# Optimization experiments

Measured on AMD Instinct MI355X. Metric: run time of the kernel, lower is better.

The kernel has to match this reference:

```python
import jax, jax.numpy as jnp
import numpy as np
from jax import lax

NT, NB, NC = 128, 256, 512
HID, EMB, NCLS, NSTEPS, POSE = 256, 128, 37, 25, 256
RNN_IN = NC + EMB + POSE + 576  # 1472, matches GRUCell input dim


def roi_align_2x2(feat, boxes):
    # feat: [C,H,W] -- image 0 only, faithful to roi_align(features, [coord], (2,2))
    # which assigns all nB boxes to batch element 0.
    # boxes: [nB,4] = (x1,y1,x2,y2), torchvision semantics (aligned=False,
    # spatial_scale=1); sampling_ratio fixed to 1 (one sample per bin center).
    C, H, W = feat.shape
    x1, y1, x2, y2 = boxes[:, 0], boxes[:, 1], boxes[:, 2], boxes[:, 3]
    bw = jnp.maximum(x2 - x1, 1.0) * 0.5  # bin width  (output 2x2)
    bh = jnp.maximum(y2 - y1, 1.0) * 0.5  # bin height
    off = jnp.array([0.5, 1.5], boxes.dtype)
    ys = y1[:, None] + off[None, :] * bh[:, None]            # [nB,2]
    xs = x1[:, None] + off[None, :] * bw[:, None]            # [nB,2]
    yy = jnp.broadcast_to(ys[:, :, None], ys.shape + (2,))   # [nB,2,2]
    xx = jnp.broadcast_to(xs[:, None, :], xs.shape[:1] + (2, 2))
    valid = (yy >= -1.0) & (yy <= H) & (xx >= -1.0) & (xx <= W)
    y = jnp.clip(yy, 0.0, H - 1.0)
    x = jnp.clip(xx, 0.0, W - 1.0)
    y0 = jnp.floor(y); x0 = jnp.floor(x)
    y0i = y0.astype(jnp.int32); x0i = x0.astype(jnp.int32)
    y1i = jnp.minimum(y0i + 1, H - 1); x1i = jnp.minimum(x0i + 1, W - 1)
    ly = y - y0; lx = x - x0; hy = 1.0 - ly; hx = 1.0 - lx
    g = lambda yi, xi: feat[:, yi, xi]                       # [C,nB,2,2]
    val = (g(y0i, x0i) * (hy * hx) + g(y0i, x1i) * (hy * lx)
           + g(y1i, x0i) * (ly * hx) + g(y1i, x1i) * (ly * lx))
    val = jnp.where(valid[None], val, 0.0)                   # [C,nB,2,2]
    return jnp.transpose(val, (1, 0, 2, 3)).reshape(val.shape[1], -1)  # [nB,4C]


def setup_inputs() -> dict:
    key = jax.random.key(0)
    ks = jax.random.split(key, 20)
    s = 0.05
    return {
        "feats": jax.random.normal(ks[0], (NT, NB, NC), jnp.float32),
        "pose": jax.random.normal(ks[1], (NB, POSE, 1, NT), jnp.float32),
        "pyr0": jax.random.normal(ks[2], (NB, 16, 16, 128), jnp.float32),
        "pyr1": jax.random.normal(ks[3], (NB, 64, 8, 64), jnp.float32),
        "pyr2": jax.random.normal(ks[4], (NB, 64, 4, 65), jnp.float32),
        "text_length": jnp.full((NB,), NSTEPS, jnp.int32),
        "text": jax.random.randint(ks[5], (NB * NSTEPS,), 0, NCLS),
        # parameters
        "i2h_w": jax.random.normal(ks[6], (HID, NC)) * s,
        "h2h_w": jax.random.normal(ks[7], (HID, HID)) * s,
        "h2h_b": jnp.zeros((HID,)),
        "score_w": jax.random.normal(ks[8], (HID,)) * s,
        "pose_w": jax.random.normal(ks[9], (4, NC + POSE)) * s,
        "pose_b": jnp.zeros((4,)),
        "gru_w_ih": jax.random.normal(ks[10], (3 * HID, RNN_IN)) * s,
        "gru_w_hh": jax.random.normal(ks[11], (3 * HID, HID)) * s,
        "gru_b_ih": jnp.zeros((3 * HID,)),
        "gru_b_hh": jnp.zeros((3 * HID,)),
        "char_emb": jax.random.normal(ks[12], (NCLS + 1, EMB)),
        "gen_w": jax.random.normal(ks[13], (NCLS, HID)) * s,
        "gen_b": jnp.zeros((NCLS,)),
    }


def reference(feats, pose, pyr0, pyr1, pyr2, text_length, text,
              i2h_w, h2h_w, h2h_b, score_w, pose_w, pose_b,
              gru_w_ih, gru_w_hh, gru_b_ih, gru_b_hh,
              char_emb, gen_w, gen_b):
    nT, nB, nC = feats.shape
    # pose.squeeze(2).permute(2,0,1) -> [nT,nB,POSE]
    pose_t = jnp.transpose(pose[:, :, 0, :], (2, 0, 1))
    feats_cat = jnp.concatenate([feats, pose_t], axis=2)       # [nT,nB,nC+POSE]
    feats_proj = jnp.einsum('tbc,hc->tbh', feats, i2h_w)       # i2h, no bias

    # targets: <start>=0 then text+1 per sample (equal lengths -> reshape)
    tgt = text.reshape(nB, NSTEPS).astype(jnp.int32) + 1
    targets = jnp.concatenate([jnp.zeros((nB, 1), jnp.int32), tgt], axis=1).T  # [NSTEPS+1,nB]

    pyramid = (pyr0, pyr1, pyr2)

    def step(hidden, tgt_row):
        emb = char_emb[tgt_row]                                # [nB,EMB]
        hp = hidden @ h2h_w.T + h2h_b                          # [nB,HID]
        e = jnp.tanh(feats_proj + hp[None]) @ score_w          # [nT,nB]
        alpha = jax.nn.softmax(e, axis=0)
        ctx = jnp.einsum('tbc,tb->bc', feats_cat, alpha)       # [nB,nC+POSE]
        coord = jax.nn.sigmoid(ctx @ pose_w.T + pose_b)        # [nB,4]
        crops = []
        for f in pyramid:
            h, w = f.shape[2], f.shape[3]
            scale = jnp.array([h, w, h, w], coord.dtype)
            coord = coord * scale                              # faithful in-loop rescale
            crops.append(roi_align_2x2(f[0], coord))           # [nB,4*C_i]
        x = jnp.concatenate([ctx, emb] + crops, axis=1)        # [nB,RNN_IN]
        gi = x @ gru_w_ih.T + gru_b_ih
        gh = hidden @ gru_w_hh.T + gru_b_hh
        ir, iz, inn = jnp.split(gi, 3, axis=1)
        hr, hz, hn = jnp.split(gh, 3, axis=1)
        r = jax.nn.sigmoid(ir + hr)
        z = jax.nn.sigmoid(iz + hz)
        n = jnp.tanh(inn + r * hn)
        h_new = (1.0 - z) * n + z * hidden
        return h_new, h_new

    hidden0 = jnp.zeros((nB, HID), feats.dtype)
    _, hs = lax.scan(step, hidden0, targets[:NSTEPS])          # [NSTEPS,nB,HID]
    # re-pack per-sample (equal lengths): [b0 t0..t24, b1 t0..t24, ...]
    new_h = jnp.transpose(hs, (1, 0, 2)).reshape(nB * NSTEPS, HID)
    probs = new_h @ gen_w.T + gen_b                            # [nB*NSTEPS,NCLS]
    return probs
```

## Files before the change

### kernel.cpp

```cpp
#include <hip/hip_runtime.h>
#include <hip/hip_bf16.h>

typedef unsigned short u16;
typedef unsigned int u32;
typedef __attribute__((ext_vector_type(8))) short short8;
typedef __attribute__((ext_vector_type(4))) float floatx4;

#define NT 128
#define NB 256
#define NC 512
#define HID 256
#define EMB 128
#define NCLS 37
#define NSTEPS 25
#define POSEC 256
#define RNN_IN 1472

__device__ __forceinline__ float b2f(u16 u) {
    union { float f; u32 i; } v; v.i = ((u32)u) << 16; return v.f;
}
__device__ __forceinline__ u16 f2b(float f) {
    union { float f; u32 i; } v; v.f = f;
    u32 x = v.i;
    return (u16)((x + 0x7fffu + ((x >> 16) & 1u)) >> 16);
}
__device__ __forceinline__ float sigm(float x) { return 1.f / (1.f + expf(-x)); }

__device__ __forceinline__ float ldf(const float* p, size_t i) { return p[i]; }
__device__ __forceinline__ float ldf(const u16* p, size_t i) { return b2f(p[i]); }

__device__ __forceinline__ short8 ld8(const u16* p) { return *(const short8*)p; }
__device__ __forceinline__ short8 ld8(const float* p) {
    float4 a = *(const float4*)p; float4 b = *(const float4*)(p + 4);
    short8 r;
    r[0] = (short)f2b(a.x); r[1] = (short)f2b(a.y); r[2] = (short)f2b(a.z); r[3] = (short)f2b(a.w);
    r[4] = (short)f2b(b.x); r[5] = (short)f2b(b.y); r[6] = (short)f2b(b.z); r[7] = (short)f2b(b.w);
    return r;
}
__device__ __forceinline__ float4 ld4(const float* p) { return *(const float4*)p; }
__device__ __forceinline__ float4 ld4(const u16* p) {
    ushort4 v = *(const ushort4*)p;
    return make_float4(b2f(v.x), b2f(v.y), b2f(v.z), b2f(v.w));
}

__global__ void probe_kernel(const void* score_w, int* flag) {
    __shared__ float red[128];
    int tid = threadIdx.x;
    const u16* p = (const u16*)score_w;
    float v = fabsf(b2f(p[tid]));
    v = (v == v && v < 1e6f) ? v : 1e6f;
    red[tid] = v;
    __syncthreads();
    for (int s2 = 64; s2 > 0; s2 >>= 1) {
        if (tid < s2) red[tid] += red[tid + s2];
        __syncthreads();
    }
    if (tid == 0) flag[0] = (red[0] < 1000.f) ? 1 : 0;
}

__global__ void conv_kernel(const void* w_ih, const void* w_hh, const void* h2h_w,
                            u16* out_ih, u16* out_hh, u16* out_h2h, const int* flagp) {
    int f = *flagp;
    int idx = blockIdx.x * blockDim.x + threadIdx.x;
    int stride = gridDim.x * blockDim.x;
    const int n_ih = 768 * RNN_IN, n_hh = 768 * HID, n_h2h = HID * HID;
    if (f) {
        const u16* a = (const u16*)w_ih; const u16* b = (const u16*)w_hh;
        const u16* c = (const u16*)h2h_w;
        for (int i = idx; i < n_ih; i += stride) out_ih[i] = a[i];
        for (int i = idx; i < n_hh; i += stride) out_hh[i] = b[i];
        for (int i = idx; i < n_h2h; i += stride) {
            int j = i >> 8, cc = i & 255;
            out_h2h[(cc >> 1) * 512 + (j << 1) + (cc & 1)] = c[i];
        }
    } else {
        const float* a = (const float*)w_ih; const float* b = (const float*)w_hh;
        const float* c = (const float*)h2h_w;
        for (int i = idx; i < n_ih; i += stride) out_ih[i] = f2b(a[i]);
        for (int i = idx; i < n_hh; i += stride) out_hh[i] = f2b(b[i]);
        for (int i = idx; i < n_h2h; i += stride) {
            int j = i >> 8, cc = i & 255;
            out_h2h[(cc >> 1) * 512 + (j << 1) + (cc & 1)] = f2b(c[i]);
        }
    }
}

template <typename T>
__device__ void pconv_body(const T* pose, u16* pt) {
    size_t n = (size_t)NB * POSEC * NT;
    size_t i = ((size_t)blockIdx.x * blockDim.x + threadIdx.x) * 4;
    size_t stride = (size_t)gridDim.x * blockDim.x * 4;
    for (; i < n; i += stride) {
        float4 v = ld4(pose + i);
        ushort4 o;
        o.x = f2b(v.x); o.y = f2b(v.y); o.z = f2b(v.z); o.w = f2b(v.w);
        *(ushort4*)(pt + i) = o;
    }
}
__global__ __launch_bounds__(256) void pconv_kernel(const void* pose, u16* pt, const int* flagp) {
    if (*flagp) pconv_body((const u16*)pose, pt);
    else        pconv_body((const float*)pose, pt);
}

template <typename T>
__device__ void trans_body(const T* feats, u16* ft) {
    int b = blockIdx.x, t0 = blockIdx.y * 8;
    #pragma unroll
    for (int half = 0; half < 2; half++) {
        int c = threadIdx.x + half * 256;
        short8 v;
        #pragma unroll
        for (int j = 0; j < 8; j++)
            v[j] = (short)f2b(ldf(feats, ((size_t)(t0 + j) * NB + b) * NC + c));
        *(short8*)(ft + ((size_t)b * NC + c) * NT + t0) = v;
    }
}
__global__ __launch_bounds__(256) void trans_kernel(const void* feats, u16* ft, const int* flagp) {
    if (*flagp) trans_body((const u16*)feats, ft);
    else        trans_body((const float*)feats, ft);
}

template <typename T>
__device__ void fp_body(const T* feats, const T* i2h_w, u16* fp) {
    __shared__ u16 As[128][40];
    __shared__ u16 Bs[128][40];
    const int tid = threadIdx.x;
    const int w = tid >> 6, lane = tid & 63;
    const int m0 = blockIdx.x * 128, n0 = blockIdx.y * 128;
    const int lr = lane & 15, kq = (lane >> 4) * 8;
    const int srow = tid >> 1, schunk = (tid & 1) * 16;

    floatx4 acc[2][8];
    #pragma unroll
    for (int i = 0; i < 2; i++)
        #pragma unroll
        for (int nt = 0; nt < 8; nt++) acc[i][nt] = (floatx4){0.f, 0.f, 0.f, 0.f};

    for (int kk = 0; kk < NC; kk += 32) {
        short8 av0 = ld8(feats + (size_t)(m0 + srow) * NC + kk + schunk);
        short8 av1 = ld8(feats + (size_t)(m0 + srow) * NC + kk + schunk + 8);
        short8 bv0 = ld8(i2h_w + (size_t)(n0 + srow) * NC + kk + schunk);
        short8 bv1 = ld8(i2h_w + (size_t)(n0 + srow) * NC + kk + schunk + 8);
        __syncthreads();
        *(short8*)&As[srow][schunk] = av0;
        *(short8*)&As[srow][schunk + 8] = av1;
        *(short8*)&Bs[srow][schunk] = bv0;
        *(short8*)&Bs[srow][schunk + 8] = bv1;
        __syncthreads();
        short8 a0 = *(const short8*)&As[w * 32 + lr][kq];
        short8 a1 = *(const short8*)&As[w * 32 + 16 + lr][kq];
        #pragma unroll
        for (int nt = 0; nt < 8; nt++) {
            short8 bf = *(const short8*)&Bs[nt * 16 + lr][kq];
            acc[0][nt] = __builtin_amdgcn_mfma_f32_16x16x32_bf16(a0, bf, acc[0][nt], 0, 0, 0);
            acc[1][nt] = __builtin_amdgcn_mfma_f32_16x16x32_bf16(a1, bf, acc[1][nt], 0, 0, 0);
        }
    }

    int rbase = (lane >> 4) * 4, col = lane & 15;
    #pragma unroll
    for (int i = 0; i < 2; i++)
        #pragma unroll
        for (int nt = 0; nt < 8; nt++)
            #pragma unroll
            for (int r = 0; r < 4; r++) {
                int m = m0 + w * 32 + i * 16 + rbase + r;
                int t = m >> 8, b = m & 255;
                fp[((size_t)b * NT + t) * HID + n0 + nt * 16 + col] = f2b(acc[i][nt][r]);
            }
}
__global__ __launch_bounds__(256) void fp_kernel(const void* feats, const void* i2h_w,
                                                 u16* fp, const int* flagp) {
    if (*flagp) fp_body((const u16*)feats, (const u16*)i2h_w, fp);
    else        fp_body((const float*)feats, (const float*)i2h_w, fp);
}

template <typename T>
__device__ __forceinline__ void do_crop(
    const T* __restrict__ f, int C, int H, int W,
    float x1, float y1, float x2, float y2,
    u16* __restrict__ xrow, int off, int tid)
{
    int n = C * 4;
    if (tid >= n) return;
    float bw = fmaxf(x2 - x1, 1.f) * 0.5f;
    float bh = fmaxf(y2 - y1, 1.f) * 0.5f;
    int c = tid >> 2, iy = (tid >> 1) & 1, ix = tid & 1;
    float yy = y1 + (0.5f + (float)iy) * bh;
    float xx = x1 + (0.5f + (float)ix) * bw;
    bool valid = (yy >= -1.f) && (yy <= (float)H) && (xx <= (float)W) && (xx >= -1.f);
    float y = fminf(fmaxf(yy, 0.f), (float)(H - 1));
    float x = fminf(fmaxf(xx, 0.f), (float)(W - 1));
    float y0f = floorf(y), x0f = floorf(x);
    int y0 = (int)y0f, x0 = (int)x0f;
    int y1i = min(y0 + 1, H - 1), x1i = min(x0 + 1, W - 1);
    float ly = y - y0f, lx = x - x0f, hy = 1.f - ly, hx = 1.f - lx;
    size_t base = (size_t)c * H * W;
    float v = ldf(f, base + y0 * W + x0) * hy * hx + ldf(f, base + y0 * W + x1i) * hy * lx
            + ldf(f, base + y1i * W + x0) * ly * hx + ldf(f, base + y1i * W + x1i) * ly * lx;
    xrow[off + tid] = f2b(valid ? v : 0.f);
}

template <typename T>
__device__ void attn_body(
    const u16* pt,
    const T* pyr0, const T* pyr1, const T* pyr2,
    const int* text,
    const T* h2h_b, const T* score_w,
    const T* pose_w, const T* pose_b, const T* char_emb,
    const u16* h2h_wT, const u16* ft, const u16* fp,
    const u16* h_prev, u16* xout, int s)
{
    const int b = blockIdx.x;
    const int tid = threadIdx.x;
    extern __shared__ float smem[];
    float* h_s    = smem;
    float* hp_s   = smem + 256;
    float* sw_s   = smem + 520;
    float* ep_s   = smem + 784;
    float* pp_s   = smem + 1808;
    float* e_s    = smem + 2832;
    float* ctx_s  = smem + 2960;
    float* coord_s= smem + 3728;
    float* red_s  = smem + 3732;

    if (tid < 256) {
        h_s[tid] = b2f(h_prev[b * HID + tid]);
    } else if (tid < 512) {
        int k = tid - 256;
        sw_s[k + (k >> 5)] = ldf(score_w, k);
    }
    __syncthreads();

    {
        int j = tid & 255, qt = tid >> 8;
        float acc = 0.f;
        const u16* wp = h2h_wT + 2 * j + (size_t)qt * 32 * 512;
        #pragma unroll 8
        for (int c2 = 0; c2 < 32; c2++) {
            u32 w2 = *(const u32*)(wp + c2 * 512);
            acc += h_s[qt * 64 + 2 * c2] * b2f((u16)w2)
                 + h_s[qt * 64 + 2 * c2 + 1] * b2f((u16)(w2 >> 16));
        }
        ep_s[tid] = acc;
    }
    __syncthreads();
    if (tid < 256) {
        float v = ep_s[tid] + ep_s[tid + 256] + ep_s[tid + 512] + ep_s[tid + 768]
                + ldf(h2h_b, tid);
        hp_s[tid + (tid >> 5)] = v;
    }
    __syncthreads();

    {
        int t = tid >> 3, q = tid & 7;
        const u16* fr = fp + ((size_t)b * NT + t) * HID + q * 32;
        int kb = q * 32;
        float acc = 0.f;
        #pragma unroll
        for (int v8 = 0; v8 < 4; v8++) {
            short8 v = *(const short8*)(fr + 8 * v8);
            #pragma unroll
            for (int j = 0; j < 8; j++) {
                int k = kb + v8 * 8 + j;
                int ki = k + (k >> 5);
                acc += tanhf(b2f((u16)v[j]) + hp_s[ki]) * sw_s[ki];
            }
        }
        ep_s[tid] = acc;
    }
    __syncthreads();
    if (tid < NT) {
        float v = 0.f;
        #pragma unroll
        for (int q = 0; q < 8; q++) v += ep_s[8 * tid + q];
        e_s[tid] = v;
    }
    __syncthreads();

    if (tid < 64) {
        float m = fmaxf(e_s[tid], e_s[tid + 64]);
        for (int off = 32; off; off >>= 1) m = fmaxf(m, __shfl_down(m, off));
        if (tid == 0) red_s[0] = m;
    }
    __syncthreads();
    float mx = red_s[0];
    if (tid < NT) e_s[tid] = expf(e_s[tid] - mx);
    __syncthreads();
    if (tid < 64) {
        float sm = e_s[tid] + e_s[tid + 64];
        for (int off = 32; off; off >>= 1) sm += __shfl_down(sm, off);
        if (tid == 0) red_s[1] = sm;
    }
    __syncthreads();
    float inv = 1.f / red_s[1];
    if (tid < NT) e_s[tid] *= inv;
    __syncthreads();

    u16* xr = xout + (size_t)b * RNN_IN;

    {
        int c = tid & 511, th = tid >> 9;
        const u16* row = ft + ((size_t)b * NC + c) * NT + th * 64;
        float acc = 0.f;
        #pragma unroll
        for (int t8 = 0; t8 < 8; t8++) {
            short8 v = *(const short8*)(row + 8 * t8);
            #pragma unroll
            for (int j = 0; j < 8; j++)
                acc += e_s[th * 64 + 8 * t8 + j] * b2f((u16)v[j]);
        }
        ep_s[tid] = acc;
    }
    {
        int p = tid & 255, qt = tid >> 8;
        const u16* row = pt + ((size_t)b * POSEC + p) * NT + qt * 32;
        float acc = 0.f;
        #pragma unroll
        for (int t8 = 0; t8 < 4; t8++) {
            short8 v = *(const short8*)(row + 8 * t8);
            #pragma unroll
            for (int j = 0; j < 8; j++)
                acc += e_s[qt * 32 + 8 * t8 + j] * b2f((u16)v[j]);
        }
        pp_s[tid] = acc;
    }
    __syncthreads();
    if (tid < 512) {
        float v = ep_s[tid] + ep_s[tid + 512];
        ctx_s[tid] = v;
        xr[tid] = f2b(v);
    } else if (tid < 768) {
        int p = tid - 512;
        float v = pp_s[p] + pp_s[p + 256] + pp_s[p + 512] + pp_s[p + 768];
        ctx_s[512 + p] = v;
        xr[512 + p] = f2b(v);
    }
    __syncthreads();

    if (tid < 256) {
        int j = tid >> 6, lane = tid & 63;
        float acc = 0.f;
        for (int c = lane; c < 768; c += 64) acc += ctx_s[c] * ldf(pose_w, (size_t)j * 768 + c);
        for (int off = 32; off; off >>= 1) acc += __shfl_down(acc, off);
        if (lane == 0) coord_s[j] = sigm(acc + ldf(pose_b, j));
    }
    __syncthreads();

    float c0 = coord_s[0], c1 = coord_s[1], c2 = coord_s[2], c3 = coord_s[3];
    if (tid < 64)
        do_crop(pyr0, 16, 16, 128, c0 * 16.f,  c1 * 128.f,    c2 * 16.f,  c3 * 128.f,    xr, 896,  tid);
    else if (tid >= 256 && tid < 512)
        do_crop(pyr1, 64, 8,  64,  c0 * 128.f, c1 * 8192.f,   c2 * 128.f, c3 * 8192.f,   xr, 960,  tid - 256);
    else if (tid >= 512 && tid < 768)
        do_crop(pyr2, 64, 4,  65,  c0 * 512.f, c1 * 532480.f, c2 * 512.f, c3 * 532480.f, xr, 1216, tid - 512);
    else if (tid >= 768 && tid < 768 + EMB) {
        int tt = tid - 768;
        int tgt = (s > 0) ? (text[b * NSTEPS + (s - 1)] + 1) : 0;
        xr[768 + tt] = f2b(ldf(char_emb, (size_t)tgt * EMB + tt));
    }
}

__global__ __launch_bounds__(1024) void attn_kernel(
    const u16* pt,
    const void* pyr0, const void* pyr1, const void* pyr2,
    const int* text,
    const void* h2h_b, const void* score_w,
    const void* pose_w, const void* pose_b, const void* char_emb,
    const u16* h2h_wT, const u16* ft, const u16* fp,
    const u16* h_prev, u16* xout, int s, const int* flagp)
{
    if (*flagp)
        attn_body(pt, (const u16*)pyr0, (const u16*)pyr1,
                  (const u16*)pyr2, text, (const u16*)h2h_b, (const u16*)score_w,
                  (const u16*)pose_w, (const u16*)pose_b, (const u16*)char_emb,
                  h2h_wT, ft, fp, h_prev, xout, s);
    else
        attn_body(pt, (const float*)pyr0, (const float*)pyr1,
                  (const float*)pyr2, text, (const float*)h2h_b, (const float*)score_w,
                  (const float*)pose_w, (const float*)pose_b, (const float*)char_emb,
                  h2h_wT, ft, fp, h_prev, xout, s);
}

template <typename T>
__device__ void gru_body(
    const u16* x, const u16* h_prev, u16* h_new,
    const u16* w_ih, const u16* w_hh, const T* b_ih, const T* b_hh)
{
    const int jt = blockIdx.x, bt = blockIdx.y;
    const int tid = threadIdx.x;
    const int w = tid >> 6, lane = tid & 63;
    const int lr = lane & 15;
    const int kq = (lane >> 4) * 8;
    const int arow = bt * 16 + lr;

    floatx4 acc_r = {0.f,0.f,0.f,0.f}, acc_z = acc_r, acc_in = acc_r, acc_hn = acc_r;

    for (int kc = w; kc < RNN_IN / 32; kc += 8) {
        int k0 = kc * 32 + kq;
        short8 a = *(const short8*)(x + (size_t)arow * RNN_IN + k0);
        short8 b0 = *(const short8*)(w_ih + (size_t)(0 * HID + jt * 16 + lr) * RNN_IN + k0);
        short8 b1 = *(const short8*)(w_ih + (size_t)(1 * HID + jt * 16 + lr) * RNN_IN + k0);
        short8 b2 = *(const short8*)(w_ih + (size_t)(2 * HID + jt * 16 + lr) * RNN_IN + k0);
        acc_r  = __builtin_amdgcn_mfma_f32_16x16x32_bf16(a, b0, acc_r, 0, 0, 0);
        acc_z  = __builtin_amdgcn_mfma_f32_16x16x32_bf16(a, b1, acc_z, 0, 0, 0);
        acc_in = __builtin_amdgcn_mfma_f32_16x16x32_bf16(a, b2, acc_in, 0, 0, 0);
    }
    for (int kc = w; kc < HID / 32; kc += 8) {
        int k0 = kc * 32 + kq;
        short8 a = *(const short8*)(h_prev + (size_t)arow * HID + k0);
        short8 b0 = *(const short8*)(w_hh + (size_t)(0 * HID + jt * 16 + lr) * HID + k0);
        short8 b1 = *(const short8*)(w_hh + (size_t)(1 * HID + jt * 16 + lr) * HID + k0);
        short8 b2 = *(const short8*)(w_hh + (size_t)(2 * HID + jt * 16 + lr) * HID + k0);
        acc_r  = __builtin_amdgcn_mfma_f32_16x16x32_bf16(a, b0, acc_r, 0, 0, 0);
        acc_z  = __builtin_amdgcn_mfma_f32_16x16x32_bf16(a, b1, acc_z, 0, 0, 0);
        acc_hn = __builtin_amdgcn_mfma_f32_16x16x32_bf16(a, b2, acc_hn, 0, 0, 0);
    }

    extern __shared__ float red[];
    int jcol = lane & 15, rb = (lane >> 4) * 4;
    #pragma unroll
    for (int r = 0; r < 4; r++) {
        red[((w * 4 + 0) * 16 + jcol) * 17 + rb + r] = acc_r[r];
        red[((w * 4 + 1) * 16 + jcol) * 17 + rb + r] = acc_z[r];
        red[((w * 4 + 2) * 16 + jcol) * 17 + rb + r] = acc_in[r];
        red[((w * 4 + 3) * 16 + jcol) * 17 + rb + r] = acc_hn[r];
    }
    __syncthreads();

    if (tid < 256) {
        int jj = tid >> 4, bl = tid & 15;
        float sr = 0, sz = 0, sin_ = 0, shn = 0;
        #pragma unroll
        for (int w2 = 0; w2 < 8; w2++) {
            sr   += red[((w2 * 4 + 0) * 16 + jj) * 17 + bl];
            sz   += red[((w2 * 4 + 1) * 16 + jj) * 17 + bl];
            sin_ += red[((w2 * 4 + 2) * 16 + jj) * 17 + bl];
            shn  += red[((w2 * 4 + 3) * 16 + jj) * 17 + bl];
        }
        int j = jt * 16 + jj, b = bt * 16 + bl;
        float r  = sigm(sr + ldf(b_ih, j) + ldf(b_hh, j));
        float zz = sigm(sz + ldf(b_ih, j + 256) + ldf(b_hh, j + 256));
        float n  = tanhf(sin_ + ldf(b_ih, j + 512) + r * (shn + ldf(b_hh, j + 512)));
        float hp = b2f(h_prev[(size_t)b * HID + j]);
        h_new[(size_t)b * HID + j] = f2b((1.f - zz) * n + zz * hp);
    }
}

__global__ __launch_bounds__(512) void gru_kernel(
    const u16* x, const u16* h_prev, u16* h_new,
    const u16* w_ih, const u16* w_hh,
    const void* b_ih, const void* b_hh, const int* flagp)
{
    if (*flagp) gru_body(x, h_prev, h_new, w_ih, w_hh, (const u16*)b_ih, (const u16*)b_hh);
    else        gru_body(x, h_prev, h_new, w_ih, w_hh, (const float*)b_ih, (const float*)b_hh);
}

template <typename T>
__device__ void gen_body(const u16* hs, const T* gen_w, const T* gen_b, void* out) {
    int rowid = blockIdx.x;
    int b = rowid / NSTEPS, s = rowid % NSTEPS;
    const u16* h = hs + ((size_t)(s + 1) * NB + b) * HID;
    extern __shared__ float hsd[];
    int tid = threadIdx.x;
    for (int i = tid; i < HID; i += 64) hsd[i] = b2f(h[i]);
    __syncthreads();
    if (tid < NCLS) {
        float acc = ldf(gen_b, tid);
        const T* wr = gen_w + (size_t)tid * HID;
        #pragma unroll 4
        for (int k4 = 0; k4 < HID / 4; k4++) {
            float4 wv = ld4(wr + 4 * k4);
            acc += hsd[4 * k4 + 0] * wv.x + hsd[4 * k4 + 1] * wv.y
                 + hsd[4 * k4 + 2] * wv.z + hsd[4 * k4 + 3] * wv.w;
        }
        size_t o = (size_t)rowid * NCLS + tid;
        if (sizeof(T) == 2) ((u16*)out)[o] = f2b(acc);
        else                ((float*)out)[o] = acc;
    }
}
__global__ __launch_bounds__(64) void gen_kernel(
    const u16* hs, const void* gen_w, const void* gen_b, void* out, const int* flagp)
{
    if (*flagp) gen_body(hs, (const u16*)gen_w, (const u16*)gen_b, out);
    else        gen_body(hs, (const float*)gen_w, (const float*)gen_b, out);
}

extern "C" void kernel_launch(void* const* d_in, const int* in_sizes, int n_in,
                              void* d_out, int out_size, void* d_ws, size_t ws_size,
                              hipStream_t stream) {
    (void)in_sizes; (void)n_in; (void)out_size;
    const int* text = (const int*)d_in[6];

    char* ws = (char*)d_ws;
    size_t off = 256;
    int* flag = (int*)ws;
    u16* fp = (u16*)(ws + off); off += (size_t)NB * NT * HID * 2;
    u16* ft = (u16*)(ws + off); off += (size_t)NB * NC * NT * 2;
    u16* hs     = (u16*)(ws + off); off += 3407872;
    u16* x      = (u16*)(ws + off); off += 753664;
    u16* wih_c  = (u16*)(ws + off); off += 2260992;
    u16* whh_c  = (u16*)(ws + off); off += 393216;
    u16* h2h_wT = (u16*)(ws + off); off += 131072;
    u16* pt     = (u16*)(ws + off); off += (size_t)NB * POSEC * NT * 2;

    probe_kernel<<<1, 128, 0, stream>>>(d_in[10], flag);
    conv_kernel<<<512, 256, 0, stream>>>(d_in[13], d_in[14], d_in[8],
                                         wih_c, whh_c, h2h_wT, flag);
    hipMemsetAsync(hs, 0, (size_t)NB * HID * 2, stream);
    fp_kernel<<<dim3(256, 2), 256, 0, stream>>>(d_in[0], d_in[7], fp, flag);
    trans_kernel<<<dim3(NB, NT / 8), 256, 0, stream>>>(d_in[0], ft, flag);
    pconv_kernel<<<2048, 256, 0, stream>>>(d_in[1], pt, flag);

    for (int s = 0; s < NSTEPS; s++) {
        attn_kernel<<<NB, 1024, 14936, stream>>>(
            pt, d_in[2], d_in[3], d_in[4], text,
            d_in[9], d_in[10], d_in[11], d_in[12], d_in[17],
            h2h_wT, ft, fp, hs + (size_t)s * NB * HID, x, s, flag);
        gru_kernel<<<dim3(16, 16), 512, 34816, stream>>>(
            x, hs + (size_t)s * NB * HID, hs + (size_t)(s + 1) * NB * HID,
            wih_c, whh_c, d_in[15], d_in[16], flag);
    }
    gen_kernel<<<NB * NSTEPS, 64, 1024, stream>>>(hs, d_in[18], d_in[19], d_out, flag);
}
```

Measured before the change: 1.252 ms.

## Batch hidden projection into MFMA kernel and restructure attention to 512 threads

```diff
diff --git a/kernel.cpp b/kernel.cpp
--- a/kernel.cpp
+++ b/kernel.cpp
@@ -25,6 +25,12 @@
     return (u16)((x + 0x7fffu + ((x >> 16) & 1u)) >> 16);
 }
 __device__ __forceinline__ float sigm(float x) { return 1.f / (1.f + expf(-x)); }
+
+__device__ __forceinline__ float ftanh(float x) {
+    float t = __expf(-2.f * fabsf(x));
+    float r = (1.f - t) * __builtin_amdgcn_rcpf(1.f + t);
+    return copysignf(r, x);
+}
 
 __device__ __forceinline__ float ldf(const float* p, size_t i) { return p[i]; }
 __device__ __forceinline__ float ldf(const u16* p, size_t i) { return b2f(p[i]); }
@@ -69,19 +75,13 @@
         const u16* c = (const u16*)h2h_w;
         for (int i = idx; i < n_ih; i += stride) out_ih[i] = a[i];
         for (int i = idx; i < n_hh; i += stride) out_hh[i] = b[i];
-        for (int i = idx; i < n_h2h; i += stride) {
-            int j = i >> 8, cc = i & 255;
-            out_h2h[(cc >> 1) * 512 + (j << 1) + (cc & 1)] = c[i];
-        }
+        for (int i = idx; i < n_h2h; i += stride) out_h2h[i] = c[i];
     } else {
         const float* a = (const float*)w_ih; const float* b = (const float*)w_hh;
         const float* c = (const float*)h2h_w;
         for (int i = idx; i < n_ih; i += stride) out_ih[i] = f2b(a[i]);
         for (int i = idx; i < n_hh; i += stride) out_hh[i] = f2b(b[i]);
-        for (int i = idx; i < n_h2h; i += stride) {
-            int j = i >> 8, cc = i & 255;
-            out_h2h[(cc >> 1) * 512 + (j << 1) + (cc & 1)] = f2b(c[i]);
-        }
+        for (int i = idx; i < n_h2h; i += stride) out_h2h[i] = f2b(c[i]);
     }
 }
 
@@ -173,6 +173,56 @@
                                                  u16* fp, const int* flagp) {
     if (*flagp) fp_body((const u16*)feats, (const u16*)i2h_w, fp);
     else        fp_body((const float*)feats, (const float*)i2h_w, fp);
+}
+
+__global__ __launch_bounds__(256) void hp_kernel(const u16* h_prev, const u16* h2h_c,
+                                                 float* hp_all) {
+    __shared__ u16 As[128][40];
+    __shared__ u16 Bs[128][40];
+    const int tid = threadIdx.x;
+    const int w = tid >> 6, lane = tid & 63;
+    const int m0 = blockIdx.x * 128, n0 = blockIdx.y * 128;
+    const int lr = lane & 15, kq = (lane >> 4) * 8;
+    const int srow = tid >> 1, schunk = (tid & 1) * 16;
+
+    floatx4 acc[2][8];
+    #pragma unroll
+    for (int i = 0; i < 2; i++)
+        #pragma unroll
+        for (int nt = 0; nt < 8; nt++) acc[i][nt] = (floatx4){0.f, 0.f, 0.f, 0.f};
+
+    for (int kk = 0; kk < HID; kk += 32) {
+        short8 av0 = *(const short8*)(h_prev + (size_t)(m0 + srow) * HID + kk + schunk);
+        short8 av1 = *(const short8*)(h_prev + (size_t)(m0 + srow) * HID + kk + schunk + 8);
+        short8 bv0 = *(const short8*)(h2h_c + (size_t)(n0 + srow) * HID + kk + schunk);
+        short8 bv1 = *(const short8*)(h2h_c + (size_t)(n0 + srow) * HID + kk + schunk + 8);
+        __syncthreads();
+        *(short8*)&As[srow][schunk] = av0;
+        *(short8*)&As[srow][schunk + 8] = av1;
+        *(short8*)&Bs[srow][schunk] = bv0;
+        *(short8*)&Bs[srow][schunk + 8] = bv1;
+        __syncthreads();
+        short8 a0 = *(const short8*)&As[w * 32 + lr][kq];
+        short8 a1 = *(const short8*)&As[w * 32 + 16 + lr][kq];
+        #pragma unroll
+        for (int nt = 0; nt < 8; nt++) {
+            short8 bf = *(const short8*)&Bs[nt * 16 + lr][kq];
+            acc[0][nt] = __builtin_amdgcn_mfma_f32_16x16x32_bf16(a0, bf, acc[0][nt], 0, 0, 0);
+            acc[1][nt] = __builtin_amdgcn_mfma_f32_16x16x32_bf16(a1, bf, acc[1][nt], 0, 0, 0);
+        }
+    }
+
+    int rbase = (lane >> 4) * 4, col = lane & 15;
+    #pragma unroll
+    for (int i = 0; i < 2; i++)
+        #pragma unroll
+        for (int nt = 0; nt < 8; nt++)
+            #pragma unroll
+            for (int r = 0; r < 4; r++) {
+                int m = m0 + w * 32 + i * 16 + rbase + r;
+                int n = n0 + nt * 16 + col;
+                hp_all[(size_t)m * HID + n] = acc[i][nt][r];
+            }
 }
 
 template <typename T>
@@ -208,178 +258,179 @@
     const int* text,
     const T* h2h_b, const T* score_w,
     const T* pose_w, const T* pose_b, const T* char_emb,
-    const u16* h2h_wT, const u16* ft, const u16* fp,
-    const u16* h_prev, u16* xout, int s)
+    const float* hp_all, const u16* ft, const u16* fp,
+    u16* xout, int s)
 {
     const int b = blockIdx.x;
     const int tid = threadIdx.x;
-    extern __shared__ float smem[];
-    float* h_s    = smem;
-    float* hp_s   = smem + 256;
-    float* sw_s   = smem + 520;
-    float* ep_s   = smem + 784;
-    float* pp_s   = smem + 1808;
-    float* e_s    = smem + 2832;
-    float* ctx_s  = smem + 2960;
-    float* coord_s= smem + 3728;
-    float* red_s  = smem + 3732;
+    __shared__ __align__(16) float smem[2452];
+    float* hp_s    = smem;
+    float* sw_s    = smem + 264;
+    float* ep_s    = smem + 528;
+    float* pp_s    = smem + 1040;
+    float* e_s     = smem + 1552;
+    float* ctx_s   = smem + 1680;
+    float* coord_s = smem + 2448;
+
+    float hpv = 0.f, swv = 0.f;
+    if (tid < 256) hpv = hp_all[(size_t)b * HID + tid] + ldf(h2h_b, tid);
+    else           swv = ldf(score_w, tid - 256);
+
+    int tgt = 0;
+    if (s > 0) tgt = text[b * NSTEPS + (s - 1)] + 1;
+    float embv = 0.f;
+    if (tid >= 256 && tid < 256 + EMB)
+        embv = ldf(char_emb, (size_t)tgt * EMB + (tid - 256));
+
+    float pwv[12];
+    {
+        int j = (tid >> 6) & 3, lane = tid & 63;
+        #pragma unroll
+        for (int k = 0; k < 12; k++)
+            pwv[k] = (tid < 256) ? ldf(pose_w, (size_t)j * 768 + k * 64 + lane) : 0.f;
+    }
+    float pbv = (tid < 256 && (tid & 63) == 0) ? ldf(pose_b, tid >> 6) : 0.f;
+
+    const int t_e = tid >> 2, q_e = tid & 3;
+    const u16* fpr = fp + ((size_t)b * NT + t_e) * HID + q_e * 64;
+    short8 fpv[8];
+    #pragma unroll
+    for (int i = 0; i < 8; i++) fpv[i] = *(const short8*)(fpr + 8 * i);
+
+    const u16* ftr = ft + ((size_t)b * NC + tid) * NT;
+    short8 ftv[16];
+    #pragma unroll
+    for (int i = 0; i < 16; i++) ftv[i] = *(const short8*)(ftr + 8 * i);
+
+    const int p_c = tid & 255, hf = tid >> 8;
+    const u16* ptr_ = pt + ((size_t)b * POSEC + p_c) * NT + hf * 64;
+    short8 ptv[8];
+    #pragma unroll
+    for (int i = 0; i < 8; i++) ptv[i] = *(const short8*)(ptr_ + 8 * i);
 
     if (tid < 256) {
-        h_s[tid] = b2f(h_prev[b * HID + tid]);
-    } else if (tid < 512) {
+        hp_s[tid + (tid >> 5)] = hpv;
+    } else {
         int k = tid - 256;
-        sw_s[k + (k >> 5)] = ldf(score_w, k);
+        sw_s[k + (k >> 5)] = swv;
     }
     __syncthreads();
 
     {
-        int j = tid & 255, qt = tid >> 8;
         float acc = 0.f;
-        const u16* wp = h2h_wT + 2 * j + (size_t)qt * 32 * 512;
-        #pragma unroll 8
-        for (int c2 = 0; c2 < 32; c2++) {
-            u32 w2 = *(const u32*)(wp + c2 * 512);
-            acc += h_s[qt * 64 + 2 * c2] * b2f((u16)w2)
-                 + h_s[qt * 64 + 2 * c2 + 1] * b2f((u16)(w2 >> 16));
-        }
-        ep_s[tid] = acc;
-    }
-    __syncthreads();
-    if (tid < 256) {
-        float v = ep_s[tid] + ep_s[tid + 256] + ep_s[tid + 512] + ep_s[tid + 768]
-                + ldf(h2h_b, tid);
-        hp_s[tid + (tid >> 5)] = v;
-    }
-    __syncthreads();
-
-    {
-        int t = tid >> 3, q = tid & 7;
-        const u16* fr = fp + ((size_t)b * NT + t) * HID + q * 32;
-        int kb = q * 32;
-        float acc = 0.f;
-        #pragma unroll
-        for (int v8 = 0; v8 < 4; v8++) {
-            short8 v = *(const short8*)(fr + 8 * v8);
+        #pragma unroll
+        for (int i = 0; i < 8; i++) {
+            short8 v = fpv[i];
             #pragma unroll
             for (int j = 0; j < 8; j++) {
-                int k = kb + v8 * 8 + j;
-                int ki = k + (k >> 5);
-                acc += tanhf(b2f((u16)v[j]) + hp_s[ki]) * sw_s[ki];
+                int h = q_e * 64 + i * 8 + j;
+                int ki = h + (h >> 5);
+                acc += ftanh(b2f((u16)v[j]) + hp_s[ki]) * sw_s[ki];
             }
         }
         ep_s[tid] = acc;
     }
     __syncthreads();
-    if (tid < NT) {
-        float v = 0.f;
-        #pragma unroll
-        for (int q = 0; q < 8; q++) v += ep_s[8 * tid + q];
-        e_s[tid] = v;
-    }
-    __syncthreads();
 
     if (tid < 64) {
-        float m = fmaxf(e_s[tid], e_s[tid + 64]);
-        for (int off = 32; off; off >>= 1) m = fmaxf(m, __shfl_down(m, off));
-        if (tid == 0) red_s[0] = m;
-    }
-    __syncthreads();
-    float mx = red_s[0];
-    if (tid < NT) e_s[tid] = expf(e_s[tid] - mx);
-    __syncthreads();
+        float4 a = *(const float4*)&ep_s[4 * tid];
+        float4 c = *(const float4*)&ep_s[4 * (tid + 64)];
+        float eL = a.x + a.y + a.z + a.w;
+        float eH = c.x + c.y + c.z + c.w;
+        float m = fmaxf(eL, eH);
+        #pragma unroll
+        for (int off = 32; off; off >>= 1) m = fmaxf(m, __shfl_xor(m, off));
+        float pL = __expf(eL - m), pH = __expf(eH - m);
+        float sm = pL + pH;
+        #pragma unroll
+        for (int off = 32; off; off >>= 1) sm += __shfl_xor(sm, off);
+        float inv = 1.f / sm;
+        e_s[tid] = pL * inv;
+        e_s[tid + 64] = pH * inv;
+    }
+    __syncthreads();
+
+    u16* xr = xout + (size_t)b * RNN_IN;
+
+    {
+        float acc = 0.f;
+        #pragma unroll
+        for (int i = 0; i < 16; i++) {
+            float4 a0 = *(const float4*)&e_s[8 * i];
+            float4 a1 = *(const float4*)&e_s[8 * i + 4];
+            short8 v = ftv[i];
+            acc += a0.x * b2f((u16)v[0]) + a0.y * b2f((u16)v[1])
+                 + a0.z * b2f((u16)v[2]) + a0.w * b2f((u16)v[3])
+                 + a1.x * b2f((u16)v[4]) + a1.y * b2f((u16)v[5])
+                 + a1.z * b2f((u16)v[6]) + a1.w * b2f((u16)v[7]);
+        }
+        ctx_s[tid] = acc;
+        xr[tid] = f2b(acc);
+    }
+    {
+        float acc = 0.f;
+        #pragma unroll
+        for (int i = 0; i < 8; i++) {
+            float4 a0 = *(const float4*)&e_s[hf * 64 + 8 * i];
+            float4 a1 = *(const float4*)&e_s[hf * 64 + 8 * i + 4];
+            short8 v = ptv[i];
+            acc += a0.x * b2f((u16)v[0]) + a0.y * b2f((u16)v[1])
+                 + a0.z * b2f((u16)v[2]) + a0.w * b2f((u16)v[3])
+                 + a1.x * b2f((u16)v[4]) + a1.y * b2f((u16)v[5])
+                 + a1.z * b2f((u16)v[6]) + a1.w * b2f((u16)v[7]);
+        }
+        pp_s[tid] = acc;
+    }
+    if (tid >= 256 && tid < 256 + EMB) xr[768 + (tid - 256)] = f2b(embv);
+    __syncthreads();
+    if (tid < 256) {
+        float v = pp_s[tid] + pp_s[tid + 256];
+        ctx_s[512 + tid] = v;
+        xr[512 + tid] = f2b(v);
+    }
+    __syncthreads();
+
+    if (tid < 256) {
+        int lane = tid & 63;
+        float acc = 0.f;
+        #pragma unroll
+        for (int k = 0; k < 12; k++) acc += ctx_s[lane + k * 64] * pwv[k];
+        #pragma unroll
+        for (int off = 32; off; off >>= 1) acc += __shfl_down(acc, off);
+        if (lane == 0) coord_s[tid >> 6] = sigm(acc + pbv);
+    }
+    __syncthreads();
+
+    float c0 = coord_s[0], c1 = coord_s[1], c2 = coord_s[2], c3 = coord_s[3];
     if (tid < 64) {
-        float sm = e_s[tid] + e_s[tid + 64];
-        for (int off = 32; off; off >>= 1) sm += __shfl_down(sm, off);
-        if (tid == 0) red_s[1] = sm;
-    }
-    __syncthreads();
-    float inv = 1.f / red_s[1];
-    if (tid < NT) e_s[tid] *= inv;
-    __syncthreads();
-
-    u16* xr = xout + (size_t)b * RNN_IN;
-
-    {
-        int c = tid & 511, th = tid >> 9;
-        const u16* row = ft + ((size_t)b * NC + c) * NT + th * 64;
-        float acc = 0.f;
-        #pragma unroll
-        for (int t8 = 0; t8 < 8; t8++) {
-            short8 v = *(const short8*)(row + 8 * t8);
-            #pragma unroll
-            for (int j = 0; j < 8; j++)
-                acc += e_s[th * 64 + 8 * t8 + j] * b2f((u16)v[j]);
-        }
-        ep_s[tid] = acc;
-    }
-    {
-        int p = tid & 255, qt = tid >> 8;
-        const u16* row = pt + ((size_t)b * POSEC + p) * NT + qt * 32;
-        float acc = 0.f;
-        #pragma unroll
-        for (int t8 = 0; t8 < 4; t8++) {
-            short8 v = *(const short8*)(row + 8 * t8);
-            #pragma unroll
-            for (int j = 0; j < 8; j++)
-                acc += e_s[qt * 32 + 8 * t8 + j] * b2f((u16)v[j]);
-        }
-        pp_s[tid] = acc;
-    }
-    __syncthreads();
-    if (tid < 512) {
-        float v = ep_s[tid] + ep_s[tid + 512];
-        ctx_s[tid] = v;
-        xr[tid] = f2b(v);
-    } else if (tid < 768) {
-        int p = tid - 512;
-        float v = pp_s[p] + pp_s[p + 256] + pp_s[p + 512] + pp_s[p + 768];
-        ctx_s[512 + p] = v;
-        xr[512 + p] = f2b(v);
-    }
-    __syncthreads();
-
-    if (tid < 256) {
-        int j = tid >> 6, lane = tid & 63;
-        float acc = 0.f;
-        for (int c = lane; c < 768; c += 64) acc += ctx_s[c] * ldf(pose_w, (size_t)j * 768 + c);
-        for (int off = 32; off; off >>= 1) acc += __shfl_down(acc, off);
-        if (lane == 0) coord_s[j] = sigm(acc + ldf(pose_b, j));
-    }
-    __syncthreads();
-
-    float c0 = coord_s[0], c1 = coord_s[1], c2 = coord_s[2], c3 = coord_s[3];
-    if (tid < 64)
         do_crop(pyr0, 16, 16, 128, c0 * 16.f,  c1 * 128.f,    c2 * 16.f,  c3 * 128.f,    xr, 896,  tid);
-    else if (tid >= 256 && tid < 512)
-        do_crop(pyr1, 64, 8,  64,  c0 * 128.f, c1 * 8192.f,   c2 * 128.f, c3 * 8192.f,   xr, 960,  tid - 256);
-    else if (tid >= 512 && tid < 768)
-        do_crop(pyr2, 64, 4,  65,  c0 * 512.f, c1 * 532480.f, c2 * 512.f, c3 * 532480.f, xr, 1216, tid - 512);
-    else if (tid >= 768 && tid < 768 + EMB) {
-        int tt = tid - 768;
-        int tgt = (s > 0) ? (text[b * NSTEPS + (s - 1)] + 1) : 0;
-        xr[768 + tt] = f2b(ldf(char_emb, (size_t)tgt * EMB + tt));
-    }
-}
-
-__global__ __launch_bounds__(1024) void attn_kernel(
+        do_crop(pyr2, 64, 4,  65,  c0 * 512.f, c1 * 532480.f, c2 * 512.f, c3 * 532480.f, xr, 1216, tid + 192);
+    } else if (tid < 320) {
+        do_crop(pyr1, 64, 8,  64,  c0 * 128.f, c1 * 8192.f,   c2 * 128.f, c3 * 8192.f,   xr, 960,  tid - 64);
+    } else {
+        do_crop(pyr2, 64, 4,  65,  c0 * 512.f, c1 * 532480.f, c2 * 512.f, c3 * 532480.f, xr, 1216, tid - 320);
+    }
+}
+
+__global__ __launch_bounds__(512, 2) void attn_kernel(
     const u16* pt,
     const void* pyr0, const void* pyr1, const void* pyr2,
     const int* text,
     const void* h2h_b, const void* score_w,
     const void* pose_w, const void* pose_b, const void* char_emb,
-    const u16* h2h_wT, const u16* ft, const u16* fp,
-    const u16* h_prev, u16* xout, int s, const int* flagp)
+    const float* hp_all, const u16* ft, const u16* fp,
+    u16* xout, int s, const int* flagp)
 {
     if (*flagp)
         attn_body(pt, (const u16*)pyr0, (const u16*)pyr1,
                   (const u16*)pyr2, text, (const u16*)h2h_b, (const u16*)score_w,
                   (const u16*)pose_w, (const u16*)pose_b, (const u16*)char_emb,
-                  h2h_wT, ft, fp, h_prev, xout, s);
+                  hp_all, ft, fp, xout, s);
     else
         attn_body(pt, (const float*)pyr0, (const float*)pyr1,
                   (const float*)pyr2, text, (const float*)h2h_b, (const float*)score_w,
                   (const float*)pose_w, (const float*)pose_b, (const float*)char_emb,
-                  h2h_wT, ft, fp, h_prev, xout, s);
+                  hp_all, ft, fp, xout, s);
 }
 
 template <typename T>
@@ -501,22 +552,24 @@
     u16* x      = (u16*)(ws + off); off += 753664;
     u16* wih_c  = (u16*)(ws + off); off += 2260992;
     u16* whh_c  = (u16*)(ws + off); off += 393216;
-    u16* h2h_wT = (u16*)(ws + off); off += 131072;
+    u16* h2h_c  = (u16*)(ws + off); off += 131072;
     u16* pt     = (u16*)(ws + off); off += (size_t)NB * POSEC * NT * 2;
+    float* hp_all = (float*)(ws + off); off += (size_t)NB * HID * 4;
 
     probe_kernel<<<1, 128, 0, stream>>>(d_in[10], flag);
     conv_kernel<<<512, 256, 0, stream>>>(d_in[13], d_in[14], d_in[8],
-                                         wih_c, whh_c, h2h_wT, flag);
+                                         wih_c, whh_c, h2h_c, flag);
     hipMemsetAsync(hs, 0, (size_t)NB * HID * 2, stream);
     fp_kernel<<<dim3(256, 2), 256, 0, stream>>>(d_in[0], d_in[7], fp, flag);
     trans_kernel<<<dim3(NB, NT / 8), 256, 0, stream>>>(d_in[0], ft, flag);
     pconv_kernel<<<2048, 256, 0, stream>>>(d_in[1], pt, flag);
 
     for (int s = 0; s < NSTEPS; s++) {
-        attn_kernel<<<NB, 1024, 14936, stream>>>(
+        hp_kernel<<<dim3(2, 2), 256, 0, stream>>>(hs + (size_t)s * NB * HID, h2h_c, hp_all);
+        attn_kernel<<<NB, 512, 0, stream>>>(
             pt, d_in[2], d_in[3], d_in[4], text,
             d_in[9], d_in[10], d_in[11], d_in[12], d_in[17],
-            h2h_wT, ft, fp, hs + (size_t)s * NB * HID, x, s, flag);
+            hp_all, ft, fp, x, s, flag);
         gru_kernel<<<dim3(16, 16), 512, 34816, stream>>>(
             x, hs + (size_t)s * NB * HID, hs + (size_t)(s + 1) * NB * HID,
             wih_c, whh_c, d_in[15], d_in[16], flag);
```

After: 1.157 ms. -7.6%, faster.
